# Performance work log

Hardware: AMD Instinct MI355X
Metric: run time of the kernel (lower is better)

The kernel has to match this reference:

```python
import jax, jax.numpy as jnp
import numpy as np

B, S, D, H, FF, L = 2, 2048, 512, 8, 2048, 2
HD = D // H
EPS = 1e-5
NEG = -1e9


def layernorm(x, gamma, beta):
    # mean/var over last axis (axis=2 in original)
    mean = jnp.mean(x, axis=-1, keepdims=True)
    var = jnp.mean((x - mean) ** 2, axis=-1, keepdims=True)
    return gamma * (x - mean) / jnp.sqrt(var + EPS) + beta


def masked_attention(x, mask, Wqkv, Wo, bo):
    b, s, d = x.shape
    qkv = x @ Wqkv                                  # [B,S,3D]
    qkv = qkv.reshape(b, s, H, 3 * HD)
    qkv = qkv.reshape(b, H, s, 3 * HD)              # original uses reshape, not transpose
    q, k, v = jnp.split(qkv, 3, axis=3)             # each [B,H,S,HD]
    scaled = jnp.einsum('bhqd,bhkd->bhqk', q, k) / (HD ** 0.5)
    col = mask[:, None, None, :]                    # valid key columns
    row = mask[:, None, :, None]                    # valid query rows
    logits = jnp.where(col, scaled, NEG)
    attn = jax.nn.softmax(logits, axis=-1)
    attn = attn * (row & col).astype(attn.dtype)    # exact zeros outside valid block
    values = jnp.einsum('bhqk,bhkd->bhqd', attn, v)  # [B,H,S,HD]
    values = values.reshape(b, s, H * HD)           # original uses reshape, not transpose
    return values @ Wo + bo


def encoder_layer(x, mask, p):
    res = x
    x = masked_attention(x, mask, p['Wqkv'], p['Wo'], p['bo'])
    x = layernorm(x + res, p['g1'], p['be1'])
    res = x
    x = jax.nn.relu(x @ p['W1'] + p['bf1']) @ p['W2'] + p['bf2']
    x = layernorm(x + res, p['g2'], p['be2'])
    return x


def setup_inputs() -> dict:
    key = jax.random.key(0)
    ks = jax.random.split(key, 8)
    x = jax.random.normal(ks[0], (B, S, D), jnp.float32)
    lengths = jax.random.randint(ks[1], (B,), S // 2, S + 1)
    paded_mask = jnp.arange(S)[None, :] < lengths[:, None]   # [B,S] bool
    sc = 0.02
    return {
        'x': x,
        'paded_mask': paded_mask,
        'Wqkv': jax.random.normal(ks[2], (L, D, 3 * D), jnp.float32) * sc,
        'Wo': jax.random.normal(ks[3], (L, D, D), jnp.float32) * sc,
        'bo': jnp.zeros((L, D), jnp.float32),
        'g1': jnp.ones((L, D), jnp.float32),
        'be1': jnp.zeros((L, D), jnp.float32),
        'W1': jax.random.normal(ks[4], (L, D, FF), jnp.float32) * sc,
        'bf1': jnp.zeros((L, FF), jnp.float32),
        'W2': jax.random.normal(ks[5], (L, FF, D), jnp.float32) * sc,
        'bf2': jnp.zeros((L, D), jnp.float32),
        'g2': jnp.ones((L, D), jnp.float32),
        'be2': jnp.zeros((L, D), jnp.float32),
    }


def reference(x, paded_mask, Wqkv, Wo, bo, g1, be1, W1, bf1, W2, bf2, g2, be2):
    for i in range(L):
        p = {'Wqkv': Wqkv[i], 'Wo': Wo[i], 'bo': bo[i], 'g1': g1[i], 'be1': be1[i],
             'W1': W1[i], 'bf1': bf1[i], 'W2': W2[i], 'bf2': bf2[i], 'g2': g2[i], 'be2': be2[i]}
        x = encoder_layer(x, paded_mask, p)
    return x
```

## Files before the change

### kernel.cpp

```cpp
#include <hip/hip_runtime.h>
#include <math.h>


typedef __bf16 bf16x8 __attribute__((ext_vector_type(8)));
typedef float f32x4 __attribute__((ext_vector_type(4)));

static constexpr int S_ = 2048;
static constexpr int D_ = 512;
static constexpr int FF_ = 2048;
static constexpr int M_ = 4096;
static constexpr int OPC_ = 2 * 8 * 2048;

__global__ __launch_bounds__(256) void transpose_cvt(
    const float* __restrict__ W, __bf16* __restrict__ Wt, int K, int N) {
  __shared__ float tile[32][33];
  const int t = threadIdx.x;
  const int tx = t & 31, ty = t >> 5;
  const size_t off = (size_t)blockIdx.z * K * N;
  const int n0 = blockIdx.x * 32, k0 = blockIdx.y * 32;
#pragma unroll
  for (int i = 0; i < 4; ++i)
    tile[ty + i * 8][tx] = W[off + (size_t)(k0 + ty + i * 8) * N + n0 + tx];
  __syncthreads();
#pragma unroll
  for (int i = 0; i < 4; ++i)
    Wt[off + (size_t)(n0 + ty + i * 8) * K + k0 + tx] = (__bf16)tile[tx][ty + i * 8];
}

template <int BM, int BN, int WM, int WN, bool A_BF16, bool OUT_BF16,
          bool RELU, bool SPLITK2>
__global__ __launch_bounds__(256) void gemm_tile(
    const void* __restrict__ Av, const __bf16* __restrict__ Wt,
    const float* __restrict__ bias, void* __restrict__ Cv,
    int M, int N, int K) {
  constexpr int BK = 64;
  constexpr int MI = BM / WM / 16;
  constexpr int NJ = BN / WN / 16;
  __shared__ __bf16 As[BM][BK + 8];
  __shared__ __bf16 Bs[BN][BK + 8];

  const int t = threadIdx.x;
  const int bm = blockIdx.x * BM, bn = blockIdx.y * BN;
  const int wv = t >> 6;
  const int ln16 = t & 15, quad = (t & 63) >> 4;
  const int wm = (wv % WM) * (BM / WM), wn = (wv / WM) * (BN / WN);

  int kbeg = 0, kend = K;
  if (SPLITK2) {
    const int half = K >> 1;
    kbeg = blockIdx.z * half;
    kend = kbeg + half;
  }

  f32x4 acc[MI][NJ];
#pragma unroll
  for (int i = 0; i < MI; ++i)
#pragma unroll
    for (int j = 0; j < NJ; ++j) acc[i][j] = {0.f, 0.f, 0.f, 0.f};

  const float* Af = (const float*)Av;
  const __bf16* Ab = (const __bf16*)Av;

  for (int k0 = kbeg; k0 < kend; k0 += BK) {
#pragma unroll
    for (int it = 0; it < BM / 32; ++it) {
      int g = t + it * 256;
      int r = g >> 3, c = (g & 7) * 8;
      if (A_BF16) {
        *(bf16x8*)&As[r][c] = *(const bf16x8*)(Ab + (size_t)(bm + r) * K + k0 + c);
      } else {
        const float* p = Af + (size_t)(bm + r) * K + k0 + c;
        float4 f0 = *(const float4*)p, f1 = *(const float4*)(p + 4);
        bf16x8 v;
        v[0] = (__bf16)f0.x; v[1] = (__bf16)f0.y; v[2] = (__bf16)f0.z; v[3] = (__bf16)f0.w;
        v[4] = (__bf16)f1.x; v[5] = (__bf16)f1.y; v[6] = (__bf16)f1.z; v[7] = (__bf16)f1.w;
        *(bf16x8*)&As[r][c] = v;
      }
    }
#pragma unroll
    for (int it = 0; it < BN / 32; ++it) {
      int g = t + it * 256;
      int r = g >> 3, c = (g & 7) * 8;
      *(bf16x8*)&Bs[r][c] = *(const bf16x8*)(Wt + (size_t)(bn + r) * K + k0 + c);
    }
    __syncthreads();
#pragma unroll
    for (int kk = 0; kk < 2; ++kk) {
      bf16x8 a[MI], b[NJ];
#pragma unroll
      for (int i = 0; i < MI; ++i)
        a[i] = *(const bf16x8*)&As[wm + i * 16 + ln16][kk * 32 + quad * 8];
#pragma unroll
      for (int j = 0; j < NJ; ++j)
        b[j] = *(const bf16x8*)&Bs[wn + j * 16 + ln16][kk * 32 + quad * 8];
#pragma unroll
      for (int i = 0; i < MI; ++i)
#pragma unroll
        for (int j = 0; j < NJ; ++j)
          acc[i][j] = __builtin_amdgcn_mfma_f32_16x16x32_bf16(a[i], b[j], acc[i][j], 0, 0, 0);
    }
    __syncthreads();
  }

  float* Cs = (float*)Cv;
  if (SPLITK2) Cs += (size_t)blockIdx.z * M * N;
  const bool addb = bias && (!SPLITK2 || blockIdx.z == 0);
#pragma unroll
  for (int i = 0; i < MI; ++i) {
#pragma unroll
    for (int j = 0; j < NJ; ++j) {
      const int col = bn + wn + j * 16 + ln16;
      const float bv = addb ? bias[col] : 0.f;
#pragma unroll
      for (int r = 0; r < 4; ++r) {
        const int row = bm + wm + i * 16 + quad * 4 + r;
        float v = acc[i][j][r] + bv;
        if (RELU) v = fmaxf(v, 0.f);
        if (OUT_BF16)
          ((__bf16*)Cv)[(size_t)row * N + col] = (__bf16)v;
        else
          Cs[(size_t)row * N + col] = v;
      }
    }
  }
}

__global__ __launch_bounds__(256) void attn_mfma(
    const __bf16* __restrict__ qkv, const int* __restrict__ mask,
    float* __restrict__ OP, float* __restrict__ LP) {
  const int b = blockIdx.z >> 1, chunk = blockIdx.z & 1;
  const int h = blockIdx.y;
  const int q0 = blockIdx.x * 64;
  const int t = threadIdx.x;
  const int wq = t >> 6, ln16 = t & 15, quad = (t & 63) >> 4;

  __shared__ __bf16 Ks[64][72];
  __shared__ __bf16 Vt[64][72];
  __shared__ __bf16 Ps[64][72];
  __shared__ int maskv[64];

  const __bf16* base = qkv + (size_t)b * S_ * 1536 + (size_t)h * S_ * 192;
  const int* mrow = mask + (size_t)b * S_;
  const int kbase = chunk * 1024, kend = kbase + 1024;

  const int r0 = t >> 3, cst = (t & 7) * 8;

  bf16x8 aq[2];
  {
    const int q = q0 + wq * 16 + ln16;
    aq[0] = *(const bf16x8*)(base + (size_t)q * 192 + quad * 8);
    aq[1] = *(const bf16x8*)(base + (size_t)q * 192 + 32 + quad * 8);
  }

  float lpart[4] = {0.f, 0.f, 0.f, 0.f};
  f32x4 o[4];
#pragma unroll
  for (int d = 0; d < 4; ++d) o[d] = {0.f, 0.f, 0.f, 0.f};

  bf16x8 kreg[2], vreg[2];
  int mreg = 1;
#pragma unroll
  for (int it = 0; it < 2; ++it) {
    int r = r0 + it * 32;
    kreg[it] = *(const bf16x8*)(base + (size_t)(kbase + r) * 192 + 64 + cst);
    vreg[it] = *(const bf16x8*)(base + (size_t)(kbase + r) * 192 + 128 + cst);
  }
  if (t < 64) mreg = mrow[kbase + t];

  for (int k0 = kbase; k0 < kend; k0 += 64) {
    if (mrow[k0] == 0) break;

#pragma unroll
    for (int it = 0; it < 2; ++it) {
      int r = r0 + it * 32;
      *(bf16x8*)&Ks[r][cst] = kreg[it];
#pragma unroll
      for (int e = 0; e < 8; ++e) Vt[cst + e][r ^ cst] = vreg[it][e];
    }
    if (t < 64) maskv[t] = mreg;
    __syncthreads();

    {
      const int kp = (k0 + 64 < kend) ? k0 + 64 : k0;
#pragma unroll
      for (int it = 0; it < 2; ++it) {
        int r = r0 + it * 32;
        kreg[it] = *(const bf16x8*)(base + (size_t)(kp + r) * 192 + 64 + cst);
        vreg[it] = *(const bf16x8*)(base + (size_t)(kp + r) * 192 + 128 + cst);
      }
      if (t < 64) mreg = mrow[kp + t];
    }

    f32x4 sf[4];
#pragma unroll
    for (int j = 0; j < 4; ++j) sf[j] = {0.f, 0.f, 0.f, 0.f};
#pragma unroll
    for (int kk = 0; kk < 2; ++kk) {
#pragma unroll
      for (int j = 0; j < 4; ++j) {
        bf16x8 bk = *(const bf16x8*)&Ks[j * 16 + ln16][kk * 32 + quad * 8];
        sf[j] = __builtin_amdgcn_mfma_f32_16x16x32_bf16(aq[kk], bk, sf[j], 0, 0, 0);
      }
    }

#pragma unroll
    for (int j = 0; j < 4; ++j) {
      const bool mv = maskv[j * 16 + ln16] != 0;
#pragma unroll
      for (int r = 0; r < 4; ++r) {
        float p = mv ? __expf(fminf(sf[j][r] * 0.125f, 60.f)) : 0.f;
        sf[j][r] = p;
        lpart[r] += p;
      }
    }

#pragma unroll
    for (int j = 0; j < 4; ++j)
#pragma unroll
      for (int r = 0; r < 4; ++r)
        Ps[wq * 16 + quad * 4 + r][j * 16 + ln16] = (__bf16)sf[j][r];
    asm volatile("s_waitcnt lgkmcnt(0)" ::: "memory");

#pragma unroll
    for (int kk = 0; kk < 2; ++kk) {
      bf16x8 pb = *(const bf16x8*)&Ps[wq * 16 + ln16][kk * 32 + quad * 8];
#pragma unroll
      for (int dt = 0; dt < 4; ++dt) {
        const int hsw = (2 * dt + (ln16 >> 3)) & 7;
        bf16x8 av = *(const bf16x8*)&Vt[dt * 16 + ln16][((4 * kk + quad) ^ hsw) * 8];
        o[dt] = __builtin_amdgcn_mfma_f32_16x16x32_bf16(av, pb, o[dt], 0, 0, 0);
      }
    }
    __syncthreads();
  }

  {
    const int q = q0 + wq * 16 + ln16;
    float* opc = OP + (size_t)chunk * OPC_ * 64 +
                 ((size_t)((b * 8 + h) * 2048) + q) * 64;
#pragma unroll
    for (int dt = 0; dt < 4; ++dt)
      *(float4*)(opc + dt * 16 + quad * 4) =
          make_float4(o[dt][0], o[dt][1], o[dt][2], o[dt][3]);
  }
#pragma unroll
  for (int off = 1; off < 16; off <<= 1)
#pragma unroll
    for (int r = 0; r < 4; ++r) lpart[r] += __shfl_xor(lpart[r], off, 64);
  if (ln16 == 0) {
#pragma unroll
    for (int r = 0; r < 4; ++r)
      LP[chunk * OPC_ + (b * 8 + h) * 2048 + q0 + wq * 16 + quad * 4 + r] = lpart[r];
  }
}

__global__ __launch_bounds__(256) void linv_kernel(
    const float* __restrict__ LP, const int* __restrict__ mask,
    float* __restrict__ Linv) {
  const int idx = blockIdx.x * 256 + threadIdx.x;
  const int b = idx >> 14, q = idx & 2047;
  const float l = LP[idx] + LP[OPC_ + idx];
  Linv[idx] = (mask[b * 2048 + q] != 0 && l > 0.f) ? 1.f / l : 0.f;
}

__global__ __launch_bounds__(256) void gemm_wo(
    const float* __restrict__ OP, const float* __restrict__ Linv,
    const __bf16* __restrict__ Wt, const float* __restrict__ bias,
    float* __restrict__ C) {
  constexpr int BK = 64;
  __shared__ __bf16 As[64][BK + 8];
  __shared__ __bf16 Bs[64][BK + 8];

  const int t = threadIdx.x;
  const int bm = blockIdx.x * 64, bn = blockIdx.y * 64;
  const int wv = t >> 6;
  const int ln16 = t & 15, quad = (t & 63) >> 4;
  const int wm = (wv & 1) * 32, wn = (wv >> 1) * 32;
  const int b = bm >> 11, qb = bm & 2047;

  f32x4 acc[2][2];
#pragma unroll
  for (int i = 0; i < 2; ++i)
#pragma unroll
    for (int j = 0; j < 2; ++j) acc[i][j] = {0.f, 0.f, 0.f, 0.f};

  for (int k0 = 0; k0 < 512; k0 += BK) {
    const int h = k0 >> 6;
    const float* O0 = OP + ((size_t)((b * 8 + h) * 2048) + qb) * 64;
    const float* lv = Linv + (b * 8 + h) * 2048 + qb;
#pragma unroll
    for (int it = 0; it < 2; ++it) {
      int r = (t >> 3) + it * 32, c = (t & 7) * 8;
      const float s = lv[r];
      const float* p0 = O0 + (size_t)r * 64 + c;
      const float* p1 = p0 + (size_t)OPC_ * 64;
      float4 a0 = *(const float4*)p0, a1 = *(const float4*)(p0 + 4);
      float4 b0 = *(const float4*)p1, b1 = *(const float4*)(p1 + 4);
      bf16x8 v;
      v[0] = (__bf16)((a0.x + b0.x) * s); v[1] = (__bf16)((a0.y + b0.y) * s);
      v[2] = (__bf16)((a0.z + b0.z) * s); v[3] = (__bf16)((a0.w + b0.w) * s);
      v[4] = (__bf16)((a1.x + b1.x) * s); v[5] = (__bf16)((a1.y + b1.y) * s);
      v[6] = (__bf16)((a1.z + b1.z) * s); v[7] = (__bf16)((a1.w + b1.w) * s);
      *(bf16x8*)&As[r][c] = v;
    }
#pragma unroll
    for (int it = 0; it < 2; ++it) {
      int g = t + it * 256;
      int r = g >> 3, c = (g & 7) * 8;
      *(bf16x8*)&Bs[r][c] = *(const bf16x8*)(Wt + (size_t)(bn + r) * 512 + k0 + c);
    }
    __syncthreads();
#pragma unroll
    for (int kk = 0; kk < 2; ++kk) {
      bf16x8 a[2], bb[2];
#pragma unroll
      for (int i = 0; i < 2; ++i)
        a[i] = *(const bf16x8*)&As[wm + i * 16 + ln16][kk * 32 + quad * 8];
#pragma unroll
      for (int j = 0; j < 2; ++j)
        bb[j] = *(const bf16x8*)&Bs[wn + j * 16 + ln16][kk * 32 + quad * 8];
#pragma unroll
      for (int i = 0; i < 2; ++i)
#pragma unroll
        for (int j = 0; j < 2; ++j)
          acc[i][j] = __builtin_amdgcn_mfma_f32_16x16x32_bf16(a[i], bb[j], acc[i][j], 0, 0, 0);
    }
    __syncthreads();
  }

#pragma unroll
  for (int i = 0; i < 2; ++i) {
#pragma unroll
    for (int j = 0; j < 2; ++j) {
      const int col = bn + wn + j * 16 + ln16;
      const float bv = bias[col];
#pragma unroll
      for (int r = 0; r < 4; ++r) {
        const int row = bm + wm + i * 16 + quad * 4 + r;
        C[(size_t)row * 512 + col] = acc[i][j][r] + bv;
      }
    }
  }
}

__global__ __launch_bounds__(256) void add_ln_kernel(
    const float* __restrict__ a, const float* __restrict__ a2,
    const float* __restrict__ res, const float* __restrict__ g,
    const float* __restrict__ be, float* __restrict__ out) {
  const int row = blockIdx.x;
  const int t = threadIdx.x;
  const float* pa = a + (size_t)row * D_;
  const float* pr = res + (size_t)row * D_;

  float2 va = *(const float2*)(pa + t * 2);
  float2 vr = *(const float2*)(pr + t * 2);
  float v0 = va.x + vr.x, v1 = va.y + vr.y;
  if (a2) {
    float2 v2 = *(const float2*)(a2 + (size_t)row * D_ + t * 2);
    v0 += v2.x;
    v1 += v2.y;
  }
  float s = v0 + v1, sq = v0 * v0 + v1 * v1;
#pragma unroll
  for (int off = 32; off > 0; off >>= 1) {
    s += __shfl_down(s, off);
    sq += __shfl_down(sq, off);
  }
  __shared__ float ls[4], lsq[4];
  __shared__ float mean_s, rstd_s;
  const int wave = t >> 6, lane = t & 63;
  if (lane == 0) { ls[wave] = s; lsq[wave] = sq; }
  __syncthreads();
  if (t == 0) {
    float Sm = ls[0] + ls[1] + ls[2] + ls[3];
    float Sq = lsq[0] + lsq[1] + lsq[2] + lsq[3];
    float mean = Sm * (1.0f / D_);
    float var = Sq * (1.0f / D_) - mean * mean;
    mean_s = mean;
    rstd_s = rsqrtf(var + 1e-5f);
  }
  __syncthreads();
  float mean = mean_s, rstd = rstd_s;
  const int c = t * 2;
  float y0 = g[c] * (v0 - mean) * rstd + be[c];
  float y1 = g[c + 1] * (v1 - mean) * rstd + be[c + 1];
  *(float2*)(out + (size_t)row * D_ + c) = make_float2(y0, y1);
}

extern "C" void kernel_launch(void* const* d_in, const int* in_sizes, int n_in,
                              void* d_out, int out_size, void* d_ws, size_t ws_size,
                              hipStream_t stream) {
  const float* x_in = (const float*)d_in[0];
  const int* mask   = (const int*)d_in[1];
  const float* Wqkv = (const float*)d_in[2];
  const float* Wo   = (const float*)d_in[3];
  const float* bo   = (const float*)d_in[4];
  const float* g1   = (const float*)d_in[5];
  const float* be1  = (const float*)d_in[6];
  const float* W1   = (const float*)d_in[7];
  const float* bf1  = (const float*)d_in[8];
  const float* W2   = (const float*)d_in[9];
  const float* bf2  = (const float*)d_in[10];
  const float* g2   = (const float*)d_in[11];
  const float* be2  = (const float*)d_in[12];
  float* out = (float*)d_out;

  char* w = (char*)d_ws;
  auto alloc = [&](size_t bytes) {
    char* p = w;
    w += (bytes + 255) & ~(size_t)255;
    return p;
  };
  __bf16* WqkvT = (__bf16*)alloc((size_t)2 * 512 * 1536 * 2);
  __bf16* WoT   = (__bf16*)alloc((size_t)2 * 512 * 512 * 2);
  __bf16* W1T   = (__bf16*)alloc((size_t)2 * 512 * 2048 * 2);
  __bf16* W2T   = (__bf16*)alloc((size_t)2 * 2048 * 512 * 2);
  __bf16* R1    = (__bf16*)alloc((size_t)M_ * FF_ * 2);
  float* R2     = (float*)alloc((size_t)2 * M_ * D_ * 4);
  float* proj   = (float*)alloc((size_t)M_ * D_ * 4);
  float* x1     = (float*)alloc((size_t)M_ * D_ * 4);
  float* xE     = (float*)alloc((size_t)M_ * D_ * 4);
  float* LP     = (float*)alloc((size_t)2 * OPC_ * 4);
  float* Linv   = (float*)alloc((size_t)OPC_ * 4);

  transpose_cvt<<<dim3(1536 / 32, 512 / 32, 2), 256, 0, stream>>>(Wqkv, WqkvT, 512, 1536);
  transpose_cvt<<<dim3(512 / 32, 512 / 32, 2), 256, 0, stream>>>(Wo, WoT, 512, 512);
  transpose_cvt<<<dim3(2048 / 32, 512 / 32, 2), 256, 0, stream>>>(W1, W1T, 512, 2048);
  transpose_cvt<<<dim3(512 / 32, 2048 / 32, 2), 256, 0, stream>>>(W2, W2T, 2048, 512);

  for (int l = 0; l < 2; ++l) {
    const float* xin = (l == 0) ? x_in : xE;
    float* xout = (l == 1) ? out : xE;
    const __bf16* WqkvT_l = WqkvT + (size_t)l * 512 * 1536;
    const __bf16* WoT_l   = WoT + (size_t)l * 512 * 512;
    const __bf16* W1T_l   = W1T + (size_t)l * 512 * 2048;
    const __bf16* W2T_l   = W2T + (size_t)l * 2048 * 512;

    gemm_tile<64, 128, 1, 4, false, true, false, false>
        <<<dim3(64, 12), 256, 0, stream>>>(xin, WqkvT_l, nullptr, R1, M_, 1536, 512);
    attn_mfma<<<dim3(S_ / 64, 8, 4), 256, 0, stream>>>(R1, mask, R2, LP);
    linv_kernel<<<dim3(OPC_ / 256), 256, 0, stream>>>(LP, mask, Linv);
    gemm_wo<<<dim3(64, 8), 256, 0, stream>>>(R2, Linv, WoT_l, bo + (size_t)l * D_, proj);
    add_ln_kernel<<<dim3(M_), 256, 0, stream>>>(proj, nullptr, xin,
                                                g1 + (size_t)l * D_,
                                                be1 + (size_t)l * D_, x1);
    gemm_tile<64, 128, 1, 4, false, true, true, false>
        <<<dim3(64, 16), 256, 0, stream>>>(x1, W1T_l, bf1 + (size_t)l * FF_, R1, M_, 2048, 512);
    gemm_tile<64, 64, 2, 2, true, false, false, true>
        <<<dim3(64, 8, 2), 256, 0, stream>>>(R1, W2T_l, bf2 + (size_t)l * D_, R2, M_, 512, 2048);
    add_ln_kernel<<<dim3(M_), 256, 0, stream>>>(R2, R2 + (size_t)M_ * D_, x1,
                                                g2 + (size_t)l * D_,
                                                be2 + (size_t)l * D_, xout);
  }
}
```

Measured before the change: 379.8 us.

## Emit transposed V from QKV GEMM, prefetch GEMM tiles, interleave attention key chunks

The QKV GEMM epilogue now also writes V already transposed into a separate bf16 buffer, so attention loads V rows with vector loads instead of scattering them element by element into shared memory. The GEMM gets register prefetch of the next K tile so global loads overlap the MFMA work. Attention computes the valid length once per block and splits keys between the two chunks by interleaving 64-key tiles, which balances work under padding. It also uses swapped MFMA operands to store P as packed vectors. The cost is an extra scattered strided write in the GEMM epilogue, a mask sum per block, and more complex indexing.

```diff
diff --git a/kernel.cpp b/kernel.cpp
--- a/kernel.cpp
+++ b/kernel.cpp
@@ -3,6 +3,7 @@
 
 
 typedef __bf16 bf16x8 __attribute__((ext_vector_type(8)));
+typedef __bf16 bf16x4 __attribute__((ext_vector_type(4)));
 typedef float f32x4 __attribute__((ext_vector_type(4)));
 
 static constexpr int S_ = 2048;
@@ -28,14 +29,16 @@
 }
 
 template <int BM, int BN, int WM, int WN, bool A_BF16, bool OUT_BF16,
-          bool RELU, bool SPLITK2>
+          bool RELU, bool SPLITK2, bool QKV>
 __global__ __launch_bounds__(256) void gemm_tile(
     const void* __restrict__ Av, const __bf16* __restrict__ Wt,
     const float* __restrict__ bias, void* __restrict__ Cv,
-    int M, int N, int K) {
+    __bf16* __restrict__ VT, int M, int N, int K) {
   constexpr int BK = 64;
   constexpr int MI = BM / WM / 16;
   constexpr int NJ = BN / WN / 16;
+  constexpr int AIT = BM / 32;
+  constexpr int BIT = BN / 32;
   __shared__ __bf16 As[BM][BK + 8];
   __shared__ __bf16 Bs[BN][BK + 8];
 
@@ -44,6 +47,7 @@
   const int wv = t >> 6;
   const int ln16 = t & 15, quad = (t & 63) >> 4;
   const int wm = (wv % WM) * (BM / WM), wn = (wv / WM) * (BN / WN);
+  const int sr = t >> 3, sc = (t & 7) * 8;
 
   int kbeg = 0, kend = K;
   if (SPLITK2) {
@@ -61,29 +65,51 @@
   const float* Af = (const float*)Av;
   const __bf16* Ab = (const __bf16*)Av;
 
+  float4 pa0[AIT], pa1[AIT];
+  bf16x8 pab[AIT], pbb[BIT];
+
+  auto fetch = [&](int k0) {
+#pragma unroll
+    for (int it = 0; it < AIT; ++it) {
+      const int r = sr + it * 32;
+      if (A_BF16) {
+        pab[it] = *(const bf16x8*)(Ab + (size_t)(bm + r) * K + k0 + sc);
+      } else {
+        const float* p = Af + (size_t)(bm + r) * K + k0 + sc;
+        pa0[it] = *(const float4*)p;
+        pa1[it] = *(const float4*)(p + 4);
+      }
+    }
+#pragma unroll
+    for (int it = 0; it < BIT; ++it) {
+      const int r = sr + it * 32;
+      pbb[it] = *(const bf16x8*)(Wt + (size_t)(bn + r) * K + k0 + sc);
+    }
+  };
+
+  fetch(kbeg);
   for (int k0 = kbeg; k0 < kend; k0 += BK) {
 #pragma unroll
-    for (int it = 0; it < BM / 32; ++it) {
-      int g = t + it * 256;
-      int r = g >> 3, c = (g & 7) * 8;
+    for (int it = 0; it < AIT; ++it) {
+      const int r = sr + it * 32;
       if (A_BF16) {
-        *(bf16x8*)&As[r][c] = *(const bf16x8*)(Ab + (size_t)(bm + r) * K + k0 + c);
+        *(bf16x8*)&As[r][sc] = pab[it];
       } else {
-        const float* p = Af + (size_t)(bm + r) * K + k0 + c;
-        float4 f0 = *(const float4*)p, f1 = *(const float4*)(p + 4);
         bf16x8 v;
-        v[0] = (__bf16)f0.x; v[1] = (__bf16)f0.y; v[2] = (__bf16)f0.z; v[3] = (__bf16)f0.w;
-        v[4] = (__bf16)f1.x; v[5] = (__bf16)f1.y; v[6] = (__bf16)f1.z; v[7] = (__bf16)f1.w;
-        *(bf16x8*)&As[r][c] = v;
-      }
-    }
-#pragma unroll
-    for (int it = 0; it < BN / 32; ++it) {
-      int g = t + it * 256;
-      int r = g >> 3, c = (g & 7) * 8;
-      *(bf16x8*)&Bs[r][c] = *(const bf16x8*)(Wt + (size_t)(bn + r) * K + k0 + c);
-    }
-    __syncthreads();
+        v[0] = (__bf16)pa0[it].x; v[1] = (__bf16)pa0[it].y;
+        v[2] = (__bf16)pa0[it].z; v[3] = (__bf16)pa0[it].w;
+        v[4] = (__bf16)pa1[it].x; v[5] = (__bf16)pa1[it].y;
+        v[6] = (__bf16)pa1[it].z; v[7] = (__bf16)pa1[it].w;
+        *(bf16x8*)&As[r][sc] = v;
+      }
+    }
+#pragma unroll
+    for (int it = 0; it < BIT; ++it)
+      *(bf16x8*)&Bs[sr + it * 32][sc] = pbb[it];
+    __syncthreads();
+
+    if (k0 + BK < kend) fetch(k0 + BK);
+
 #pragma unroll
     for (int kk = 0; kk < 2; ++kk) {
       bf16x8 a[MI], b[NJ];
@@ -105,29 +131,43 @@
   float* Cs = (float*)Cv;
   if (SPLITK2) Cs += (size_t)blockIdx.z * M * N;
   const bool addb = bias && (!SPLITK2 || blockIdx.z == 0);
+  const int bidx = bm >> 11;
 #pragma unroll
   for (int i = 0; i < MI; ++i) {
 #pragma unroll
     for (int j = 0; j < NJ; ++j) {
       const int col = bn + wn + j * 16 + ln16;
-      const float bv = addb ? bias[col] : 0.f;
-#pragma unroll
-      for (int r = 0; r < 4; ++r) {
-        const int row = bm + wm + i * 16 + quad * 4 + r;
-        float v = acc[i][j][r] + bv;
-        if (RELU) v = fmaxf(v, 0.f);
-        if (OUT_BF16)
-          ((__bf16*)Cv)[(size_t)row * N + col] = (__bf16)v;
-        else
-          Cs[(size_t)row * N + col] = v;
+      if (QKV && (col % 192) >= 128) {
+        const int d = col % 192 - 128;
+        const int n8 = col / 192;
+#pragma unroll
+        for (int r = 0; r < 4; ++r) {
+          const int s = (bm + wm + i * 16 + quad * 4 + r) & 2047;
+          const int h = s >> 8;
+          const int s2 = ((s & 255) << 3) | n8;
+          VT[(((size_t)(bidx * 8 + h) * 64 + d) << 11) + s2] = (__bf16)acc[i][j][r];
+        }
+      } else {
+        const float bv = addb ? bias[col] : 0.f;
+#pragma unroll
+        for (int r = 0; r < 4; ++r) {
+          const int row = bm + wm + i * 16 + quad * 4 + r;
+          float v = acc[i][j][r] + bv;
+          if (RELU) v = fmaxf(v, 0.f);
+          if (OUT_BF16)
+            ((__bf16*)Cv)[(size_t)row * N + col] = (__bf16)v;
+          else
+            Cs[(size_t)row * N + col] = v;
+        }
       }
     }
   }
 }
 
 __global__ __launch_bounds__(256) void attn_mfma(
-    const __bf16* __restrict__ qkv, const int* __restrict__ mask,
-    float* __restrict__ OP, float* __restrict__ LP) {
+    const __bf16* __restrict__ qkv, const __bf16* __restrict__ VT,
+    const int* __restrict__ mask, float* __restrict__ OP,
+    float* __restrict__ LP) {
   const int b = blockIdx.z >> 1, chunk = blockIdx.z & 1;
   const int h = blockIdx.y;
   const int q0 = blockIdx.x * 64;
@@ -137,13 +177,25 @@
   __shared__ __bf16 Ks[64][72];
   __shared__ __bf16 Vt[64][72];
   __shared__ __bf16 Ps[64][72];
-  __shared__ int maskv[64];
+  __shared__ int lred[4];
+  __shared__ int len_sh;
 
   const __bf16* base = qkv + (size_t)b * S_ * 1536 + (size_t)h * S_ * 192;
-  const int* mrow = mask + (size_t)b * S_;
-  const int kbase = chunk * 1024, kend = kbase + 1024;
-
-  const int r0 = t >> 3, cst = (t & 7) * 8;
+  const __bf16* vbase = VT + ((size_t)(b * 8 + h) << 17);
+
+  {
+    int c = 0;
+    const int* mp = mask + b * S_ + t * 8;
+#pragma unroll
+    for (int i = 0; i < 8; ++i) c += mp[i];
+#pragma unroll
+    for (int off = 32; off >= 1; off >>= 1) c += __shfl_down(c, off, 64);
+    if ((t & 63) == 0) lred[t >> 6] = c;
+  }
+  __syncthreads();
+  if (t == 0) len_sh = lred[0] + lred[1] + lred[2] + lred[3];
+  __syncthreads();
+  const int len = len_sh;
 
   bf16x8 aq[2];
   {
@@ -152,44 +204,35 @@
     aq[1] = *(const bf16x8*)(base + (size_t)q * 192 + 32 + quad * 8);
   }
 
-  float lpart[4] = {0.f, 0.f, 0.f, 0.f};
+  float lpart = 0.f;
   f32x4 o[4];
 #pragma unroll
   for (int d = 0; d < 4; ++d) o[d] = {0.f, 0.f, 0.f, 0.f};
 
+  const int kr = t >> 3, kc = (t & 7) * 8;
+  const int vd = t >> 2, vc = (t & 3) * 16;
+  const int vphys = vc ^ ((vd & 3) * 16);
+
   bf16x8 kreg[2], vreg[2];
-  int mreg = 1;
-#pragma unroll
-  for (int it = 0; it < 2; ++it) {
-    int r = r0 + it * 32;
-    kreg[it] = *(const bf16x8*)(base + (size_t)(kbase + r) * 192 + 64 + cst);
-    vreg[it] = *(const bf16x8*)(base + (size_t)(kbase + r) * 192 + 128 + cst);
-  }
-  if (t < 64) mreg = mrow[kbase + t];
-
-  for (int k0 = kbase; k0 < kend; k0 += 64) {
-    if (mrow[k0] == 0) break;
-
-#pragma unroll
-    for (int it = 0; it < 2; ++it) {
-      int r = r0 + it * 32;
-      *(bf16x8*)&Ks[r][cst] = kreg[it];
-#pragma unroll
-      for (int e = 0; e < 8; ++e) Vt[cst + e][r ^ cst] = vreg[it][e];
-    }
-    if (t < 64) maskv[t] = mreg;
-    __syncthreads();
-
-    {
-      const int kp = (k0 + 64 < kend) ? k0 + 64 : k0;
-#pragma unroll
-      for (int it = 0; it < 2; ++it) {
-        int r = r0 + it * 32;
-        kreg[it] = *(const bf16x8*)(base + (size_t)(kp + r) * 192 + 64 + cst);
-        vreg[it] = *(const bf16x8*)(base + (size_t)(kp + r) * 192 + 128 + cst);
-      }
-      if (t < 64) mreg = mrow[kp + t];
-    }
+  auto fetch = [&](int kt) {
+    kreg[0] = *(const bf16x8*)(base + (size_t)(kt + kr) * 192 + 64 + kc);
+    kreg[1] = *(const bf16x8*)(base + (size_t)(kt + kr + 32) * 192 + 64 + kc);
+    const __bf16* vp = vbase + (size_t)vd * 2048 + kt + vc;
+    vreg[0] = *(const bf16x8*)vp;
+    vreg[1] = *(const bf16x8*)(vp + 8);
+  };
+
+  const int kbeg = chunk * 64;
+  fetch(kbeg);
+
+  for (int k0 = kbeg; k0 < len; k0 += 128) {
+    *(bf16x8*)&Ks[kr][kc] = kreg[0];
+    *(bf16x8*)&Ks[kr + 32][kc] = kreg[1];
+    *(bf16x8*)&Vt[vd][vphys] = vreg[0];
+    *(bf16x8*)&Vt[vd][vphys + 8] = vreg[1];
+    __syncthreads();
+
+    { const int kp = (k0 + 128 < S_) ? k0 + 128 : k0; fetch(kp); }
 
     f32x4 sf[4];
 #pragma unroll
@@ -198,27 +241,23 @@
     for (int kk = 0; kk < 2; ++kk) {
 #pragma unroll
       for (int j = 0; j < 4; ++j) {
-        bf16x8 bk = *(const bf16x8*)&Ks[j * 16 + ln16][kk * 32 + quad * 8];
-        sf[j] = __builtin_amdgcn_mfma_f32_16x16x32_bf16(aq[kk], bk, sf[j], 0, 0, 0);
+        bf16x8 ak = *(const bf16x8*)&Ks[j * 16 + ln16][kk * 32 + quad * 8];
+        sf[j] = __builtin_amdgcn_mfma_f32_16x16x32_bf16(ak, aq[kk], sf[j], 0, 0, 0);
       }
     }
 
 #pragma unroll
     for (int j = 0; j < 4; ++j) {
-      const bool mv = maskv[j * 16 + ln16] != 0;
+      bf16x4 pk;
 #pragma unroll
       for (int r = 0; r < 4; ++r) {
-        float p = mv ? __expf(fminf(sf[j][r] * 0.125f, 60.f)) : 0.f;
-        sf[j][r] = p;
-        lpart[r] += p;
-      }
-    }
-
-#pragma unroll
-    for (int j = 0; j < 4; ++j)
-#pragma unroll
-      for (int r = 0; r < 4; ++r)
-        Ps[wq * 16 + quad * 4 + r][j * 16 + ln16] = (__bf16)sf[j][r];
+        const float e = __expf(fminf(sf[j][r] * 0.125f, 60.f));
+        const float p = (k0 + j * 16 + quad * 4 + r < len) ? e : 0.f;
+        lpart += p;
+        pk[r] = (__bf16)p;
+      }
+      *(bf16x4*)&Ps[wq * 16 + ln16][j * 16 + quad * 4] = pk;
+    }
     asm volatile("s_waitcnt lgkmcnt(0)" ::: "memory");
 
 #pragma unroll
@@ -226,32 +265,25 @@
       bf16x8 pb = *(const bf16x8*)&Ps[wq * 16 + ln16][kk * 32 + quad * 8];
 #pragma unroll
       for (int dt = 0; dt < 4; ++dt) {
-        const int hsw = (2 * dt + (ln16 >> 3)) & 7;
-        bf16x8 av = *(const bf16x8*)&Vt[dt * 16 + ln16][((4 * kk + quad) ^ hsw) * 8];
+        bf16x8 av = *(const bf16x8*)
+            &Vt[dt * 16 + ln16][(kk * 32 + quad * 8) ^ ((ln16 & 3) * 16)];
         o[dt] = __builtin_amdgcn_mfma_f32_16x16x32_bf16(av, pb, o[dt], 0, 0, 0);
       }
     }
     __syncthreads();
   }
 
-  {
-    const int q = q0 + wq * 16 + ln16;
-    float* opc = OP + (size_t)chunk * OPC_ * 64 +
-                 ((size_t)((b * 8 + h) * 2048) + q) * 64;
-#pragma unroll
-    for (int dt = 0; dt < 4; ++dt)
-      *(float4*)(opc + dt * 16 + quad * 4) =
-          make_float4(o[dt][0], o[dt][1], o[dt][2], o[dt][3]);
-  }
-#pragma unroll
-  for (int off = 1; off < 16; off <<= 1)
-#pragma unroll
-    for (int r = 0; r < 4; ++r) lpart[r] += __shfl_xor(lpart[r], off, 64);
-  if (ln16 == 0) {
-#pragma unroll
-    for (int r = 0; r < 4; ++r)
-      LP[chunk * OPC_ + (b * 8 + h) * 2048 + q0 + wq * 16 + quad * 4 + r] = lpart[r];
-  }
+  lpart += __shfl_xor(lpart, 16, 64);
+  lpart += __shfl_xor(lpart, 32, 64);
+
+  const int q = q0 + wq * 16 + ln16;
+  float* opc = OP + (size_t)chunk * OPC_ * 64 +
+               ((size_t)((b * 8 + h) * 2048) + q) * 64;
+#pragma unroll
+  for (int dt = 0; dt < 4; ++dt)
+    *(float4*)(opc + dt * 16 + quad * 4) =
+        make_float4(o[dt][0], o[dt][1], o[dt][2], o[dt][3]);
+  if (quad == 0) LP[chunk * OPC_ + (b * 8 + h) * 2048 + q] = lpart;
 }
 
 __global__ __launch_bounds__(256) void linv_kernel(
@@ -416,6 +448,7 @@
   __bf16* W1T   = (__bf16*)alloc((size_t)2 * 512 * 2048 * 2);
   __bf16* W2T   = (__bf16*)alloc((size_t)2 * 2048 * 512 * 2);
   __bf16* R1    = (__bf16*)alloc((size_t)M_ * FF_ * 2);
+  __bf16* VTb   = (__bf16*)alloc((size_t)16 * 64 * 2048 * 2);
   float* R2     = (float*)alloc((size_t)2 * M_ * D_ * 4);
   float* proj   = (float*)alloc((size_t)M_ * D_ * 4);
   float* x1     = (float*)alloc((size_t)M_ * D_ * 4);
@@ -436,18 +469,18 @@
     const __bf16* W1T_l   = W1T + (size_t)l * 512 * 2048;
     const __bf16* W2T_l   = W2T + (size_t)l * 2048 * 512;
 
-    gemm_tile<64, 128, 1, 4, false, true, false, false>
-        <<<dim3(64, 12), 256, 0, stream>>>(xin, WqkvT_l, nullptr, R1, M_, 1536, 512);
-    attn_mfma<<<dim3(S_ / 64, 8, 4), 256, 0, stream>>>(R1, mask, R2, LP);
+    gemm_tile<64, 128, 1, 4, false, true, false, false, true>
+        <<<dim3(64, 12), 256, 0, stream>>>(xin, WqkvT_l, nullptr, R1, VTb, M_, 1536, 512);
+    attn_mfma<<<dim3(S_ / 64, 8, 4), 256, 0, stream>>>(R1, VTb, mask, R2, LP);
     linv_kernel<<<dim3(OPC_ / 256), 256, 0, stream>>>(LP, mask, Linv);
     gemm_wo<<<dim3(64, 8), 256, 0, stream>>>(R2, Linv, WoT_l, bo + (size_t)l * D_, proj);
     add_ln_kernel<<<dim3(M_), 256, 0, stream>>>(proj, nullptr, xin,
                                                 g1 + (size_t)l * D_,
                                                 be1 + (size_t)l * D_, x1);
-    gemm_tile<64, 128, 1, 4, false, true, true, false>
-        <<<dim3(64, 16), 256, 0, stream>>>(x1, W1T_l, bf1 + (size_t)l * FF_, R1, M_, 2048, 512);
-    gemm_tile<64, 64, 2, 2, true, false, false, true>
-        <<<dim3(64, 8, 2), 256, 0, stream>>>(R1, W2T_l, bf2 + (size_t)l * D_, R2, M_, 512, 2048);
+    gemm_tile<64, 128, 1, 4, false, true, true, false, false>
+        <<<dim3(64, 16), 256, 0, stream>>>(x1, W1T_l, bf1 + (size_t)l * FF_, R1, nullptr, M_, 2048, 512);
+    gemm_tile<64, 64, 2, 2, true, false, false, true, false>
+        <<<dim3(64, 8, 2), 256, 0, stream>>>(R1, W2T_l, bf2 + (size_t)l * D_, R2, nullptr, M_, 512, 2048);
     add_ln_kernel<<<dim3(M_), 256, 0, stream>>>(R2, R2 + (size_t)M_ * D_, x1,
                                                 g2 + (size_t)l * D_,
                                                 be2 + (size_t)l * D_, xout);
```

Result: faster. 353.8 us (-6.9%).
